# Performance work log

Hardware: AMD Instinct MI355X
Metric: run time of the kernel (lower is better)

The kernel has to match this reference:

```python
import jax, jax.numpy as jnp
import numpy as np

N_NODES = 50000
N_EDGES = 800000
NEG_SLOPE = 0.2  # PyG GATConv default negative_slope


def gat_conv(x, W, att_src, att_dst, bias, src, dst, heads, out_ch, concat):
    """PyG GATConv (eval mode, self-loops already appended to src/dst)."""
    n = x.shape[0]
    xh = (x @ W).reshape(n, heads, out_ch)            # [N,H,C]
    a_s = jnp.einsum('nhc,hc->nh', xh, att_src)       # [N,H]
    a_d = jnp.einsum('nhc,hc->nh', xh, att_dst)
    e = a_s[src] + a_d[dst]                           # [E,H]
    e = jnp.where(e > 0, e, NEG_SLOPE * e)            # LeakyReLU
    # segment softmax over incoming edges of each target node (dst)
    m = jax.ops.segment_max(e, dst, num_segments=n)
    e = jnp.exp(e - m[dst])
    denom = jax.ops.segment_sum(e, dst, num_segments=n)
    alpha = e / (denom[dst] + 1e-16)                  # [E,H]
    msg = xh[src] * alpha[:, :, None]                 # [E,H,C]
    out = jax.ops.segment_sum(msg, dst, num_segments=n)  # [N,H,C]
    out = out.reshape(n, heads * out_ch) if concat else out.mean(axis=1)
    return out + bias


def setup_inputs() -> dict:
    key = jax.random.key(0)
    ks = jax.random.split(key, 16)
    x = jax.random.normal(ks[0], (N_NODES, 256), dtype=jnp.float32)
    edge_index = jax.random.randint(ks[1], (2, N_EDGES), 0, N_NODES, dtype=jnp.int32)
    s = 0.05
    return {
        'x': x, 'edge_index': edge_index,
        'W0': jax.random.normal(ks[2], (256, 256), jnp.float32) * s,
        'as0': jax.random.normal(ks[3], (4, 64), jnp.float32) * s,
        'ad0': jax.random.normal(ks[4], (4, 64), jnp.float32) * s,
        'b0': jnp.zeros((256,), jnp.float32),
        'W1': jax.random.normal(ks[5], (256, 256), jnp.float32) * s,
        'as1': jax.random.normal(ks[6], (4, 64), jnp.float32) * s,
        'ad1': jax.random.normal(ks[7], (4, 64), jnp.float32) * s,
        'b1': jnp.zeros((256,), jnp.float32),
        'W2': jax.random.normal(ks[8], (256, 256), jnp.float32) * s,
        'as2': jax.random.normal(ks[9], (1, 256), jnp.float32) * s,
        'ad2': jax.random.normal(ks[10], (1, 256), jnp.float32) * s,
        'b2': jnp.zeros((256,), jnp.float32),
    }


def reference(x, edge_index, W0, as0, ad0, b0, W1, as1, ad1, b1, W2, as2, ad2, b2):
    # PyG GATConv adds self-loops by default
    loops = jnp.arange(x.shape[0], dtype=edge_index.dtype)
    src = jnp.concatenate([edge_index[0], loops])
    dst = jnp.concatenate([edge_index[1], loops])
    h = jax.nn.elu(gat_conv(x, W0, as0, ad0, b0, src, dst, 4, 64, True))
    h = jax.nn.elu(gat_conv(h, W1, as1, ad1, b1, src, dst, 4, 64, True))
    return gat_conv(h, W2, as2, ad2, b2, src, dst, 1, 256, False)
```

## Files before the change

kernel.cpp:

```cpp
#include <hip/hip_runtime.h>
#include <hip/hip_bf16.h>
#include <hip/hip_fp16.h>

#define N_NODES 50000
#define N_EDGES 800000
#define E_TOTAL (N_EDGES + N_NODES)
#define BKT 96
#define NTILES 782
#define XCAST_BLK (N_NODES * 256 / 8 / 256)
#define EDGE_BLK ((E_TOTAL + 255) / 256)

typedef _Float16 f16x8 __attribute__((ext_vector_type(8)));
typedef _Float16 f16x4 __attribute__((ext_vector_type(4)));
typedef float f32x4 __attribute__((ext_vector_type(4)));

__device__ __forceinline__ void gl_lds16(const _Float16* g, _Float16* l) {
  __builtin_amdgcn_global_load_lds(
      (const __attribute__((address_space(1))) unsigned int*)g,
      (__attribute__((address_space(3))) unsigned int*)l, 16, 0, 0);
}

__global__ __launch_bounds__(256) void prep_kernel(
    const float* __restrict__ W0, const float* __restrict__ W1,
    const float* __restrict__ W2, const float* __restrict__ x,
    const int* __restrict__ ei, _Float16* __restrict__ WT0,
    _Float16* __restrict__ WT1, _Float16* __restrict__ WT2,
    _Float16* __restrict__ X16, int* __restrict__ cursor,
    unsigned short* __restrict__ csr_src) {
  __shared__ float tile[32][33];
  const int bid = blockIdx.x;
  if (bid < 192) {
    const float* W = (bid < 64) ? W0 : (bid < 128) ? W1 : W2;
    _Float16* WT = (bid < 64) ? WT0 : (bid < 128) ? WT1 : WT2;
    const int sub = bid & 63;
    const int bx = (sub & 7) * 32, by = (sub >> 3) * 32;
    const int tx = threadIdx.x & 31, ty = threadIdx.x >> 5;
#pragma unroll
    for (int i = 0; i < 32; i += 8)
      tile[ty + i][tx] = W[(size_t)(by + ty + i) * 256 + bx + tx];
    __syncthreads();
#pragma unroll
    for (int i = 0; i < 32; i += 8)
      WT[(size_t)(bx + ty + i) * 256 + by + tx] = (_Float16)tile[tx][ty + i];
  } else if (bid < 192 + XCAST_BLK) {
    size_t i = ((size_t)(bid - 192) * 256 + threadIdx.x) * 8;
    float4 u0 = *(const float4*)(x + i);
    float4 u1 = *(const float4*)(x + i + 4);
    f16x8 v;
    v[0] = (_Float16)u0.x; v[1] = (_Float16)u0.y;
    v[2] = (_Float16)u0.z; v[3] = (_Float16)u0.w;
    v[4] = (_Float16)u1.x; v[5] = (_Float16)u1.y;
    v[6] = (_Float16)u1.z; v[7] = (_Float16)u1.w;
    *(f16x8*)(X16 + i) = v;
  } else {
    int e = (bid - 192 - XCAST_BLK) * 256 + threadIdx.x;
    if (e < E_TOTAL) {
      int s, d;
      if (e < N_EDGES) {
        s = ei[e];
        d = ei[N_EDGES + e];
      } else {
        s = d = e - N_EDGES;
      }
      int pos = atomicAdd(&cursor[d], 1);
      csr_src[(size_t)d * BKT + pos] = (unsigned short)s;
    }
  }
}

template <int H>
__global__ __launch_bounds__(256) void gemm_att(
    const _Float16* __restrict__ A, const _Float16* __restrict__ WT,
    const float* __restrict__ att_s, const float* __restrict__ att_d,
    _Float16* __restrict__ C, float* __restrict__ a_s, float* __restrict__ a_d,
    int M) {
  __shared__ _Float16 As[2][64 * 32];
  __shared__ _Float16 Bs[2][256 * 32];
  const int t = threadIdx.x, lane = t & 63, w = t >> 6;
  const int wr = w & 1, wc = w >> 1;
  const int row0 = blockIdx.x * 64;
  const int fr = lane & 15, fg = lane >> 4;
  const int srow = lane >> 2, sk = (lane & 3) * 8;

  f32x4 acc[2][8] = {};
  int cur = 0;

#define STAGE(buf, k0)                                                        \
  do {                                                                        \
    gl_lds16(A + (size_t)(row0 + w * 16 + srow) * 256 + (k0) + sk,            \
             &As[buf][w * 512]);                                              \
    gl_lds16(WT + (size_t)(w * 64 + srow) * 256 + (k0) + sk,                  \
             &Bs[buf][w * 2048]);                                             \
    gl_lds16(WT + (size_t)(w * 64 + 16 + srow) * 256 + (k0) + sk,             \
             &Bs[buf][w * 2048 + 512]);                                       \
    gl_lds16(WT + (size_t)(w * 64 + 32 + srow) * 256 + (k0) + sk,             \
             &Bs[buf][w * 2048 + 1024]);                                      \
    gl_lds16(WT + (size_t)(w * 64 + 48 + srow) * 256 + (k0) + sk,             \
             &Bs[buf][w * 2048 + 1536]);                                      \
  } while (0)

  STAGE(0, 0);
  __syncthreads();

  for (int kt = 0; kt < 8; kt++) {
    if (kt < 7) STAGE(cur ^ 1, (kt + 1) * 32);
    f16x8 af[2], bf[8];
#pragma unroll
    for (int mi = 0; mi < 2; mi++)
      af[mi] = *(const f16x8*)&As[cur][(wr * 32 + mi * 16 + fr) * 32 + fg * 8];
#pragma unroll
    for (int ni = 0; ni < 8; ni++)
      bf[ni] = *(const f16x8*)&Bs[cur][(wc * 128 + ni * 16 + fr) * 32 + fg * 8];
#pragma unroll
    for (int mi = 0; mi < 2; mi++)
#pragma unroll
      for (int ni = 0; ni < 8; ni++)
        acc[mi][ni] = __builtin_amdgcn_mfma_f32_16x16x32_f16(af[mi], bf[ni], acc[mi][ni], 0, 0, 0);
    __syncthreads();
    cur ^= 1;
  }
#undef STAGE

  float as_c[8], ad_c[8];
#pragma unroll
  for (int ni = 0; ni < 8; ni++) {
    int c = wc * 128 + ni * 16 + fr;
    as_c[ni] = att_s[c];
    ad_c[ni] = att_d[c];
  }

#pragma unroll
  for (int mi = 0; mi < 2; mi++) {
#pragma unroll
    for (int reg = 0; reg < 4; reg++) {
      const int r = row0 + wr * 32 + mi * 16 + fg * 4 + reg;
      const bool valid = r < M;
      if (valid) {
#pragma unroll
        for (int ni = 0; ni < 8; ni++)
          C[(size_t)r * 256 + wc * 128 + ni * 16 + fr] = (_Float16)acc[mi][ni][reg];
      }
      float s0 = 0.f, s1 = 0.f, d0 = 0.f, d1 = 0.f;
#pragma unroll
      for (int ni = 0; ni < 4; ni++) {
        s0 = fmaf(acc[mi][ni][reg], as_c[ni], s0);
        d0 = fmaf(acc[mi][ni][reg], ad_c[ni], d0);
        s1 = fmaf(acc[mi][ni + 4][reg], as_c[ni + 4], s1);
        d1 = fmaf(acc[mi][ni + 4][reg], ad_c[ni + 4], d1);
      }
#pragma unroll
      for (int off = 1; off < 16; off <<= 1) {
        s0 += __shfl_xor(s0, off, 64);
        d0 += __shfl_xor(d0, off, 64);
        s1 += __shfl_xor(s1, off, 64);
        d1 += __shfl_xor(d1, off, 64);
      }
      if constexpr (H == 4) {
        if (fr == 0 && valid) {
          a_s[(size_t)r * 4 + wc * 2 + 0] = s0;
          a_s[(size_t)r * 4 + wc * 2 + 1] = s1;
          a_d[(size_t)r * 4 + wc * 2 + 0] = d0;
          a_d[(size_t)r * 4 + wc * 2 + 1] = d1;
        }
      } else {
        if (fr == 0) {
          float* L = (float*)As;
          L[(r - row0) * 4 + wc * 2 + 0] = s0 + s1;
          L[(r - row0) * 4 + wc * 2 + 1] = d0 + d1;
        }
      }
    }
  }
  if constexpr (H == 1) {
    __syncthreads();
    float* L = (float*)As;
    if (t < 64 && row0 + t < M) {
      a_s[row0 + t] = L[t * 4 + 0] + L[t * 4 + 2];
      a_d[row0 + t] = L[t * 4 + 1] + L[t * 4 + 3];
    }
  }
}

template <int H, bool ELU_OUT, bool OUT_F16>
__global__ __launch_bounds__(256, 8) void aggregate_kernel(
    const _Float16* __restrict__ XH16, const float* __restrict__ a_s,
    const float* __restrict__ a_d, const int* __restrict__ cursor,
    const unsigned short* __restrict__ csr_src, const float* __restrict__ bias,
    void* __restrict__ outp) {
  const int t = threadIdx.x;
  const int lane = t & 63, w = t >> 6;
  const int d = blockIdx.x * 4 + w;
  const size_t e0 = (size_t)d * BKT;
  const int deg = cursor[d];
  const int li = lane & 15;
  const int h4 = (H == 4) ? (lane >> 4) : 0;
  const float adv = (H == 4) ? a_d[(size_t)d * 4 + h4] : a_d[d];

  float dnp = 0.f;
  float acc0 = 0.f, acc1 = 0.f, acc2 = 0.f, acc3 = 0.f;
  for (int base = 0; base < deg; base += 16) {
    const int cnt = min(16, deg - base);
    int s_cur = 0;
    float p = 0.f;
    if (li < cnt) {
      s_cur = csr_src[e0 + base + li];
      float e = ((H == 4) ? a_s[(size_t)s_cur * 4 + h4] : a_s[s_cur]) + adv;
      e = e > 0.f ? e : 0.2f * e;
      p = __expf(e);
    }
    dnp += p;
#define GAT_BODY(j)                                                           \
  {                                                                           \
    int sj = __builtin_amdgcn_readfirstlane(__shfl(s_cur, (j), 64));          \
    float alj = __shfl(p, (lane & 48) + (j), 64);                             \
    f16x4 raw = *(const f16x4*)(XH16 + (size_t)sj * 256 + lane * 4);          \
    acc0 = fmaf(alj, (float)raw[0], acc0);                                    \
    acc1 = fmaf(alj, (float)raw[1], acc1);                                    \
    acc2 = fmaf(alj, (float)raw[2], acc2);                                    \
    acc3 = fmaf(alj, (float)raw[3], acc3);                                    \
  }
    if (cnt == 16) {
#pragma unroll
      for (int j = 0; j < 16; j++) GAT_BODY(j)
    } else {
      for (int j = 0; j < cnt; j++) GAT_BODY(j)
    }
#undef GAT_BODY
  }
#pragma unroll
  for (int off = 1; off < 16; off <<= 1) dnp += __shfl_xor(dnp, off, 64);
  const float inv = 1.f / (dnp + 1e-16f);

  float4 bv = *(const float4*)&bias[lane * 4];
  float v0 = fmaf(acc0, inv, bv.x), v1 = fmaf(acc1, inv, bv.y);
  float v2 = fmaf(acc2, inv, bv.z), v3 = fmaf(acc3, inv, bv.w);
  if constexpr (ELU_OUT) {
    v0 = v0 > 0.f ? v0 : (__expf(v0) - 1.f);
    v1 = v1 > 0.f ? v1 : (__expf(v1) - 1.f);
    v2 = v2 > 0.f ? v2 : (__expf(v2) - 1.f);
    v3 = v3 > 0.f ? v3 : (__expf(v3) - 1.f);
  }
  if constexpr (OUT_F16) {
    _Float16* out = (_Float16*)outp;
    f16x4 ov;
    ov[0] = (_Float16)v0; ov[1] = (_Float16)v1;
    ov[2] = (_Float16)v2; ov[3] = (_Float16)v3;
    *(f16x4*)(out + (size_t)d * 256 + lane * 4) = ov;
  } else {
    float* out = (float*)outp;
    *(float4*)(out + (size_t)d * 256 + lane * 4) = make_float4(v0, v1, v2, v3);
  }
}

extern "C" void kernel_launch(void* const* d_in, const int* in_sizes, int n_in,
                              void* d_out, int out_size, void* d_ws, size_t ws_size,
                              hipStream_t stream) {
  const float* x = (const float*)d_in[0];
  const int* ei = (const int*)d_in[1];
  const float* W0 = (const float*)d_in[2];
  const float* as0 = (const float*)d_in[3];
  const float* ad0 = (const float*)d_in[4];
  const float* b0 = (const float*)d_in[5];
  const float* W1 = (const float*)d_in[6];
  const float* as1 = (const float*)d_in[7];
  const float* ad1 = (const float*)d_in[8];
  const float* b1 = (const float*)d_in[9];
  const float* W2 = (const float*)d_in[10];
  const float* as2 = (const float*)d_in[11];
  const float* ad2 = (const float*)d_in[12];
  const float* b2 = (const float*)d_in[13];
  float* out = (float*)d_out;

  char* p = (char*)d_ws;
  _Float16* XH16 = (_Float16*)p;
  p += (size_t)N_NODES * 256 * 2;
  _Float16* H16 = (_Float16*)p;
  p += (size_t)N_NODES * 256 * 2;
  _Float16* WT0 = (_Float16*)p;
  p += 256 * 256 * 2;
  _Float16* WT1 = (_Float16*)p;
  p += 256 * 256 * 2;
  _Float16* WT2 = (_Float16*)p;
  p += 256 * 256 * 2;
  float* a_s = (float*)p;
  p += (size_t)N_NODES * 4 * 4;
  float* a_d = (float*)p;
  p += (size_t)N_NODES * 4 * 4;
  int* cursor = (int*)p;
  p += (size_t)N_NODES * 4;
  unsigned short* csr_src = (unsigned short*)p;
  p += (size_t)N_NODES * BKT * 2;

  hipMemsetAsync(cursor, 0, (size_t)N_NODES * 4, stream);

  prep_kernel<<<192 + XCAST_BLK + EDGE_BLK, 256, 0, stream>>>(
      W0, W1, W2, x, ei, WT0, WT1, WT2, H16, cursor, csr_src);

  const int ngrid = N_NODES / 4;

  gemm_att<4><<<NTILES, 256, 0, stream>>>(H16, WT0, as0, ad0, XH16, a_s, a_d, N_NODES);
  aggregate_kernel<4, true, true><<<ngrid, 256, 0, stream>>>(
      XH16, a_s, a_d, cursor, csr_src, b0, H16);
  gemm_att<4><<<NTILES, 256, 0, stream>>>(H16, WT1, as1, ad1, XH16, a_s, a_d, N_NODES);
  aggregate_kernel<4, true, true><<<ngrid, 256, 0, stream>>>(
      XH16, a_s, a_d, cursor, csr_src, b1, H16);
  gemm_att<1><<<NTILES, 256, 0, stream>>>(H16, WT2, as2, ad2, XH16, a_s, a_d, N_NODES);
  aggregate_kernel<1, false, false><<<ngrid, 256, 0, stream>>>(
      XH16, a_s, a_d, cursor, csr_src, b2, out);
}
```

Baseline: 354.7 us.

## Fuse fp32-to-fp16 input cast into first GEMM and split prep kernel

The separate pass that converted x from fp32 to fp16 is removed. The first GEMM now loads fp32 rows into registers, converts them and writes them to LDS inside its double-buffered loop, which saves a full write and re-read of the fp16 copy of x. The weight transpose and the CSR edge scatter become two separate kernels, and the scatter uses a nontemporal store. The cost is register staging for the A tile in the first GEMM in place of direct global-to-LDS loads, and one extra kernel launch.

```diff
diff --git a/kernel.cpp b/kernel.cpp
--- a/kernel.cpp
+++ b/kernel.cpp
@@ -7,7 +7,6 @@
 #define E_TOTAL (N_EDGES + N_NODES)
 #define BKT 96
 #define NTILES 782
-#define XCAST_BLK (N_NODES * 256 / 8 / 256)
 #define EDGE_BLK ((E_TOTAL + 255) / 256)
 
 typedef _Float16 f16x8 __attribute__((ext_vector_type(8)));
@@ -22,73 +21,63 @@
 
 __global__ __launch_bounds__(256) void prep_kernel(
     const float* __restrict__ W0, const float* __restrict__ W1,
-    const float* __restrict__ W2, const float* __restrict__ x,
-    const int* __restrict__ ei, _Float16* __restrict__ WT0,
-    _Float16* __restrict__ WT1, _Float16* __restrict__ WT2,
-    _Float16* __restrict__ X16, int* __restrict__ cursor,
-    unsigned short* __restrict__ csr_src) {
+    const float* __restrict__ W2, _Float16* __restrict__ WT0,
+    _Float16* __restrict__ WT1, _Float16* __restrict__ WT2) {
   __shared__ float tile[32][33];
   const int bid = blockIdx.x;
-  if (bid < 192) {
-    const float* W = (bid < 64) ? W0 : (bid < 128) ? W1 : W2;
-    _Float16* WT = (bid < 64) ? WT0 : (bid < 128) ? WT1 : WT2;
-    const int sub = bid & 63;
-    const int bx = (sub & 7) * 32, by = (sub >> 3) * 32;
-    const int tx = threadIdx.x & 31, ty = threadIdx.x >> 5;
-#pragma unroll
-    for (int i = 0; i < 32; i += 8)
-      tile[ty + i][tx] = W[(size_t)(by + ty + i) * 256 + bx + tx];
-    __syncthreads();
-#pragma unroll
-    for (int i = 0; i < 32; i += 8)
-      WT[(size_t)(bx + ty + i) * 256 + by + tx] = (_Float16)tile[tx][ty + i];
-  } else if (bid < 192 + XCAST_BLK) {
-    size_t i = ((size_t)(bid - 192) * 256 + threadIdx.x) * 8;
-    float4 u0 = *(const float4*)(x + i);
-    float4 u1 = *(const float4*)(x + i + 4);
-    f16x8 v;
-    v[0] = (_Float16)u0.x; v[1] = (_Float16)u0.y;
-    v[2] = (_Float16)u0.z; v[3] = (_Float16)u0.w;
-    v[4] = (_Float16)u1.x; v[5] = (_Float16)u1.y;
-    v[6] = (_Float16)u1.z; v[7] = (_Float16)u1.w;
-    *(f16x8*)(X16 + i) = v;
+  const float* W = (bid < 64) ? W0 : (bid < 128) ? W1 : W2;
+  _Float16* WT = (bid < 64) ? WT0 : (bid < 128) ? WT1 : WT2;
+  const int sub = bid & 63;
+  const int bx = (sub & 7) * 32, by = (sub >> 3) * 32;
+  const int tx = threadIdx.x & 31, ty = threadIdx.x >> 5;
+#pragma unroll
+  for (int i = 0; i < 32; i += 8)
+    tile[ty + i][tx] = W[(size_t)(by + ty + i) * 256 + bx + tx];
+  __syncthreads();
+#pragma unroll
+  for (int i = 0; i < 32; i += 8)
+    WT[(size_t)(bx + ty + i) * 256 + by + tx] = (_Float16)tile[tx][ty + i];
+}
+
+__global__ __launch_bounds__(256) void scatter_kernel(
+    const int* __restrict__ ei, int* __restrict__ cursor,
+    unsigned short* __restrict__ csr_src) {
+  int e = blockIdx.x * 256 + threadIdx.x;
+  if (e >= E_TOTAL) return;
+  int s, d;
+  if (e < N_EDGES) {
+    s = ei[e];
+    d = ei[N_EDGES + e];
   } else {
-    int e = (bid - 192 - XCAST_BLK) * 256 + threadIdx.x;
-    if (e < E_TOTAL) {
-      int s, d;
-      if (e < N_EDGES) {
-        s = ei[e];
-        d = ei[N_EDGES + e];
-      } else {
-        s = d = e - N_EDGES;
-      }
-      int pos = atomicAdd(&cursor[d], 1);
-      csr_src[(size_t)d * BKT + pos] = (unsigned short)s;
-    }
-  }
-}
-
-template <int H>
+    s = d = e - N_EDGES;
+  }
+  int pos = atomicAdd(&cursor[d], 1);
+  __builtin_nontemporal_store((unsigned short)s, &csr_src[(size_t)d * BKT + pos]);
+}
+
+template <int H, bool AF16>
 __global__ __launch_bounds__(256) void gemm_att(
-    const _Float16* __restrict__ A, const _Float16* __restrict__ WT,
+    const void* __restrict__ Ap, const _Float16* __restrict__ WT,
     const float* __restrict__ att_s, const float* __restrict__ att_d,
     _Float16* __restrict__ C, float* __restrict__ a_s, float* __restrict__ a_d,
     int M) {
   __shared__ _Float16 As[2][64 * 32];
   __shared__ _Float16 Bs[2][256 * 32];
+  const _Float16* A16 = (const _Float16*)Ap;
+  const float* A32 = (const float*)Ap;
   const int t = threadIdx.x, lane = t & 63, w = t >> 6;
   const int wr = w & 1, wc = w >> 1;
   const int row0 = blockIdx.x * 64;
   const int fr = lane & 15, fg = lane >> 4;
   const int srow = lane >> 2, sk = (lane & 3) * 8;
+  const int arow = t >> 2, ak = (t & 3) * 8;
 
   f32x4 acc[2][8] = {};
   int cur = 0;
-
-#define STAGE(buf, k0)                                                        \
+  float4 ar0, ar1;
+
+#define STAGE_B(buf, k0)                                                      \
   do {                                                                        \
-    gl_lds16(A + (size_t)(row0 + w * 16 + srow) * 256 + (k0) + sk,            \
-             &As[buf][w * 512]);                                              \
     gl_lds16(WT + (size_t)(w * 64 + srow) * 256 + (k0) + sk,                  \
              &Bs[buf][w * 2048]);                                             \
     gl_lds16(WT + (size_t)(w * 64 + 16 + srow) * 256 + (k0) + sk,             \
@@ -99,11 +88,46 @@
              &Bs[buf][w * 2048 + 1536]);                                      \
   } while (0)
 
-  STAGE(0, 0);
+#define STAGE_A16(buf, k0)                                                    \
+  gl_lds16(A16 + (size_t)(row0 + w * 16 + srow) * 256 + (k0) + sk,            \
+           &As[buf][w * 512])
+
+#define LOAD_A32(k0)                                                          \
+  do {                                                                        \
+    if (row0 + arow < M) {                                                    \
+      ar0 = *(const float4*)(A32 + (size_t)(row0 + arow) * 256 + (k0) + ak);  \
+      ar1 = *(const float4*)(A32 + (size_t)(row0 + arow) * 256 + (k0) + ak + 4);\
+    } else {                                                                  \
+      ar0 = make_float4(0.f, 0.f, 0.f, 0.f);                                  \
+      ar1 = make_float4(0.f, 0.f, 0.f, 0.f);                                  \
+    }                                                                         \
+  } while (0)
+
+#define WRITE_A32(buf)                                                        \
+  do {                                                                        \
+    f16x8 v;                                                                  \
+    v[0] = (_Float16)ar0.x; v[1] = (_Float16)ar0.y;                           \
+    v[2] = (_Float16)ar0.z; v[3] = (_Float16)ar0.w;                           \
+    v[4] = (_Float16)ar1.x; v[5] = (_Float16)ar1.y;                           \
+    v[6] = (_Float16)ar1.z; v[7] = (_Float16)ar1.w;                           \
+    *(f16x8*)&As[buf][arow * 32 + ak] = v;                                    \
+  } while (0)
+
+  if constexpr (AF16) {
+    STAGE_A16(0, 0);
+  } else {
+    LOAD_A32(0);
+    WRITE_A32(0);
+  }
+  STAGE_B(0, 0);
   __syncthreads();
 
   for (int kt = 0; kt < 8; kt++) {
-    if (kt < 7) STAGE(cur ^ 1, (kt + 1) * 32);
+    if (kt < 7) {
+      if constexpr (AF16) STAGE_A16(cur ^ 1, (kt + 1) * 32);
+      else LOAD_A32((kt + 1) * 32);
+      STAGE_B(cur ^ 1, (kt + 1) * 32);
+    }
     f16x8 af[2], bf[8];
 #pragma unroll
     for (int mi = 0; mi < 2; mi++)
@@ -116,10 +140,16 @@
 #pragma unroll
       for (int ni = 0; ni < 8; ni++)
         acc[mi][ni] = __builtin_amdgcn_mfma_f32_16x16x32_f16(af[mi], bf[ni], acc[mi][ni], 0, 0, 0);
+    if constexpr (!AF16) {
+      if (kt < 7) WRITE_A32(cur ^ 1);
+    }
     __syncthreads();
     cur ^= 1;
   }
-#undef STAGE
+#undef STAGE_B
+#undef STAGE_A16
+#undef LOAD_A32
+#undef WRITE_A32
 
   float as_c[8], ad_c[8];
 #pragma unroll
@@ -293,18 +323,18 @@
 
   hipMemsetAsync(cursor, 0, (size_t)N_NODES * 4, stream);
 
-  prep_kernel<<<192 + XCAST_BLK + EDGE_BLK, 256, 0, stream>>>(
-      W0, W1, W2, x, ei, WT0, WT1, WT2, H16, cursor, csr_src);
+  prep_kernel<<<192, 256, 0, stream>>>(W0, W1, W2, WT0, WT1, WT2);
+  scatter_kernel<<<EDGE_BLK, 256, 0, stream>>>(ei, cursor, csr_src);
 
   const int ngrid = N_NODES / 4;
 
-  gemm_att<4><<<NTILES, 256, 0, stream>>>(H16, WT0, as0, ad0, XH16, a_s, a_d, N_NODES);
+  gemm_att<4, false><<<NTILES, 256, 0, stream>>>(x, WT0, as0, ad0, XH16, a_s, a_d, N_NODES);
   aggregate_kernel<4, true, true><<<ngrid, 256, 0, stream>>>(
       XH16, a_s, a_d, cursor, csr_src, b0, H16);
-  gemm_att<4><<<NTILES, 256, 0, stream>>>(H16, WT1, as1, ad1, XH16, a_s, a_d, N_NODES);
+  gemm_att<4, true><<<NTILES, 256, 0, stream>>>(H16, WT1, as1, ad1, XH16, a_s, a_d, N_NODES);
   aggregate_kernel<4, true, true><<<ngrid, 256, 0, stream>>>(
       XH16, a_s, a_d, cursor, csr_src, b1, H16);
-  gemm_att<1><<<NTILES, 256, 0, stream>>>(H16, WT2, as2, ad2, XH16, a_s, a_d, N_NODES);
+  gemm_att<1, true><<<NTILES, 256, 0, stream>>>(H16, WT2, as2, ad2, XH16, a_s, a_d, N_NODES);
   aggregate_kernel<1, false, false><<<ngrid, 256, 0, stream>>>(
       XH16, a_s, a_d, cursor, csr_src, b2, out);
 }
```

After: 354.8 us. Within noise of the previous version (+0.0%).
